# Kernel tuning notes

Measured on AMD Instinct MI355X. Metric: run time of the kernel, lower is better.

Reference implementation:

```python
import jax, jax.numpy as jnp
import numpy as np

N = 100000
E = 800000
D_IN = 256
D_H = 512


def setup_inputs() -> dict:
    key = jax.random.key(0)
    ks = jax.random.split(key, 8)
    s_in = 1.0 / np.sqrt(D_IN)
    s_h = 1.0 / np.sqrt(D_H)
    return {
        "x": jax.random.normal(ks[0], (N, D_IN), jnp.float32),
        "edge_index": jax.random.randint(ks[1], (2, E), 0, N, dtype=jnp.int64),
        "W1": jax.random.normal(ks[2], (D_IN, D_H), jnp.float32) * s_in,
        "b1": jnp.zeros((D_H,), jnp.float32),
        "W2": jax.random.normal(ks[3], (D_H, D_H), jnp.float32) * s_h,
        "b2": jnp.zeros((D_H,), jnp.float32),
        "W3": jax.random.normal(ks[4], (D_H, D_H), jnp.float32) * s_h,
        "b3": jnp.zeros((D_H,), jnp.float32),
        "Wfc": jax.random.normal(ks[5], (D_H, D_IN), jnp.float32) * s_h,
        "bfc": jnp.zeros((D_IN,), jnp.float32),
    }


def _gcn_prep(edge_index, n_nodes):
    # PyG GCNConv: add self-loops, symmetric deg^{-1/2} normalization.
    loop = jnp.arange(n_nodes, dtype=edge_index.dtype)
    row = jnp.concatenate([edge_index[0], loop])  # destination
    col = jnp.concatenate([edge_index[1], loop])  # source
    deg = jax.ops.segment_sum(jnp.ones_like(row, dtype=jnp.float32), row,
                              num_segments=n_nodes)
    dinv = jax.lax.rsqrt(deg)  # deg >= 1 due to self loops
    norm = dinv[row] * dinv[col]  # [E+N]
    return row, col, norm


def _gcn_conv(x, W, b, row, col, norm, n_nodes):
    h = x @ W  # [N, out]
    msg = h[col] * norm[:, None]  # [E+N, out] gather + scale
    out = jax.ops.segment_sum(msg, row, num_segments=n_nodes)  # scatter-add
    return out + b


def reference(x, edge_index, W1, b1, W2, b2, W3, b3, Wfc, bfc):
    n = x.shape[0]
    row, col, norm = _gcn_prep(edge_index, n)
    h = jax.nn.relu(_gcn_conv(x, W1, b1, row, col, norm, n))
    h = jax.nn.relu(_gcn_conv(h, W2, b2, row, col, norm, n))
    h = jax.nn.relu(_gcn_conv(h, W3, b3, row, col, norm, n))
    return h @ Wfc + bfc
```

## Files before the change

### kernel.cpp

```cpp
#include <hip/hip_runtime.h>

#define N_NODES 100000
#define NPAD    100096
#define E_EDGES 800000

typedef _Float16 f16;
typedef _Float16 f16x4 __attribute__((ext_vector_type(4)));
typedef _Float16 f16x8 __attribute__((ext_vector_type(8)));
typedef float    f32x4 __attribute__((ext_vector_type(4)));

__device__ inline void async16(const void* g, void* l) {
    __builtin_amdgcn_global_load_lds(
        (const __attribute__((address_space(1))) void*)g,
        (__attribute__((address_space(3))) void*)l, 16, 0, 0);
}

__global__ void k_deg(const int* __restrict__ ei, int* __restrict__ deg) {
    int e = blockIdx.x * 256 + threadIdx.x;
    if (e < E_EDGES) atomicAdd(&deg[ei[e]], 1);
}

__global__ void k_scan1(const int* __restrict__ deg, int* __restrict__ off,
                        int* __restrict__ bsum, float* __restrict__ dinv) {
    __shared__ int s[256];
    int i = blockIdx.x * 256 + threadIdx.x;
    int d = (i < N_NODES) ? deg[i] : 0;
    int pd = (d + 3) & ~3;
    dinv[i] = (i < N_NODES) ? rsqrtf((float)(d + 1)) : 0.f;
    s[threadIdx.x] = pd;
    __syncthreads();
    for (int dd = 1; dd < 256; dd <<= 1) {
        int t = (threadIdx.x >= dd) ? s[threadIdx.x - dd] : 0;
        __syncthreads();
        s[threadIdx.x] += t;
        __syncthreads();
    }
    if (i < N_NODES) off[i] = s[threadIdx.x] - pd;
    if (threadIdx.x == 255) bsum[blockIdx.x] = s[255];
}

__global__ void k_scan2(int* __restrict__ bsum, int nb) {
    __shared__ int s[512];
    int tid = threadIdx.x;
    int v = (tid < nb) ? bsum[tid] : 0;
    s[tid] = v;
    __syncthreads();
    for (int d = 1; d < 512; d <<= 1) {
        int t = (tid >= d) ? s[tid - d] : 0;
        __syncthreads();
        s[tid] += t;
        __syncthreads();
    }
    if (tid < nb) bsum[tid] = s[tid] - v;
}

__global__ void k_scan3(int* __restrict__ off, const int* __restrict__ bsum,
                        const int* __restrict__ deg, int* __restrict__ csr) {
    int i = blockIdx.x * 256 + threadIdx.x;
    if (i >= N_NODES) return;
    int o = off[i] + bsum[blockIdx.x];
    off[i] = o;
    int d = deg[i], pd = (d + 3) & ~3;
    for (int k = d; k < pd; ++k) csr[o + k] = NPAD;
    if (i == N_NODES - 1) off[N_NODES] = o + pd;
}

__global__ void k_fill(const int* __restrict__ ei, const int* __restrict__ off,
                       int* __restrict__ cursor, int* __restrict__ csr) {
    int e = blockIdx.x * 256 + threadIdx.x;
    if (e >= E_EDGES) return;
    int dst = ei[e];
    int src = ei[E_EDGES + e];
    int pos = atomicAdd(&cursor[dst], 1);
    csr[off[dst] + pos] = src;
}

__global__ void k_x_to_f16(const float* __restrict__ x,
                           const float* __restrict__ dinv,
                           f16* __restrict__ xh) {
    int i = blockIdx.x * 256 + threadIdx.x;
    if (i >= N_NODES * 64) return;
    float d = dinv[i >> 6];
    float4 v = ((const float4*)x)[i];
    f16x4 o;
    o.x = (f16)(v.x * d); o.y = (f16)(v.y * d);
    o.z = (f16)(v.z * d); o.w = (f16)(v.w * d);
    ((f16x4*)xh)[i] = o;
}

__global__ void k_transpose(const float* __restrict__ W, f16* __restrict__ Wt,
                            int K, int M) {
    int m = blockIdx.x * 256 + threadIdx.x;
    int k = blockIdx.y;
    if (m < M) Wt[(size_t)m * K + k] = (f16)W[(size_t)k * M + m];
}

template<int K, int M, int MODE>
__launch_bounds__(256, 3)
__global__ void k_gemm(const f16* __restrict__ A, const f16* __restrict__ B,
                       void* __restrict__ C, const float* __restrict__ bias,
                       const float* __restrict__ dsc) {
    __shared__ __align__(16) char smem[16384];
    f16* As = (f16*)smem;
    f16* Bs = (f16*)(smem + 8192);
    int tid  = threadIdx.x;
    int wave = tid >> 6, lane = tid & 63;
    int wr = (wave >> 1) * 64, wc = (wave & 1) * 64;
    int lm = lane & 15, q = lane >> 4;

    constexpr int CB  = M / 128;
    constexpr int NWG = (NPAD / 128) * CB;
    constexpr int Q   = NWG / 8, R = NWG % 8;
    int id  = blockIdx.x;
    int xcd = id & 7, pos = id >> 3;
    int nid = (xcd < R) ? xcd * (Q + 1) + pos
                        : R * (Q + 1) + (xcd - R) * Q + pos;
    int rowBase = (nid / CB) * 128;
    int colBase = (nid % CB) * 128;

    f32x4 acc[4][4] = {};
    const f16* Ag = A + (size_t)rowBase * K;
    const f16* Bg = B + (size_t)colBase * K;

    int c0 = tid, c1 = tid + 256;
    for (int kt = 0; kt < K; kt += 32) {
        __syncthreads();
        async16(Ag + (size_t)(c0 >> 2) * K + kt + (c0 & 3) * 8, &As[c0 * 8]);
        async16(Ag + (size_t)(c1 >> 2) * K + kt + (c1 & 3) * 8, &As[c1 * 8]);
        async16(Bg + (size_t)(c0 >> 2) * K + kt + (c0 & 3) * 8, &Bs[c0 * 8]);
        async16(Bg + (size_t)(c1 >> 2) * K + kt + (c1 & 3) * 8, &Bs[c1 * 8]);
        __syncthreads();

        f16x8 a[4], b[4];
#pragma unroll
        for (int i = 0; i < 4; ++i) {
            a[i] = *(const f16x8*)&As[(wr + i * 16 + lm) * 32 + q * 8];
            b[i] = *(const f16x8*)&Bs[(wc + i * 16 + lm) * 32 + q * 8];
        }
#pragma unroll
        for (int i = 0; i < 4; ++i)
#pragma unroll
            for (int j = 0; j < 4; ++j)
                acc[i][j] = __builtin_amdgcn_mfma_f32_16x16x32_f16(
                    a[i], b[j], acc[i][j], 0, 0, 0);
    }

    if (MODE == 2) {
#pragma unroll
        for (int i = 0; i < 4; ++i) {
            int gr0 = rowBase + wr + i * 16 + q * 4;
#pragma unroll
            for (int j = 0; j < 4; ++j) {
                int gc = colBase + wc + j * 16 + lm;
                float bj = bias[gc];
#pragma unroll
                for (int r = 0; r < 4; ++r) {
                    int gr = gr0 + r;
                    if (gr < N_NODES)
                        ((float*)C)[(size_t)gr * M + gc] = acc[i][j][r] + bj;
                }
            }
        }
    } else {
        __syncthreads();
        f16* Ep = (f16*)smem + wave * (16 * 80);
#pragma unroll
        for (int i = 0; i < 4; ++i) {
            f32x4 dr = {1.f, 1.f, 1.f, 1.f};
            if (MODE == 3)
                dr = *(const f32x4*)&dsc[rowBase + wr + i * 16 + q * 4];
#pragma unroll
            for (int j = 0; j < 4; ++j) {
                int colg = colBase + wc + j * 16 + lm;
#pragma unroll
                for (int r = 0; r < 4; ++r) {
                    float v = acc[i][j][r];
                    if (MODE == 1) {
                        v += bias[colg];
                        v = v > 0.f ? v : 0.f;
                    }
                    if (MODE == 3) v *= dr[r];
                    Ep[(q * 4 + r) * 80 + j * 16 + lm] = (f16)v;
                }
            }
            int row0 = lane >> 3, c8 = lane & 7;
            f16x8 v0 = *(const f16x8*)&Ep[row0 * 80 + c8 * 8];
            f16x8 v1 = *(const f16x8*)&Ep[(row0 + 8) * 80 + c8 * 8];
            int gr0 = rowBase + wr + i * 16 + row0;
            int gc  = colBase + wc + c8 * 8;
            *(f16x8*)&((f16*)C)[(size_t)gr0 * M + gc] = v0;
            *(f16x8*)&((f16*)C)[(size_t)(gr0 + 8) * M + gc] = v1;
        }
    }
}

template<int VE> struct VecT;
template<> struct VecT<4> { typedef f16x4 type; };
template<> struct VecT<8> { typedef f16x8 type; };

template<int CH, bool ACT>
__launch_bounds__(256)
__global__ void k_agg(const f16* __restrict__ t, const int* __restrict__ off,
                      const int* __restrict__ csr, const float* __restrict__ dinv,
                      const float* __restrict__ bias, f16* __restrict__ h) {
    constexpr int VE = CH / 64;
    typedef typename VecT<VE>::type vec;
    int node = blockIdx.x * 4 + (threadIdx.x >> 6);
    if (node >= N_NODES) return;
    int lane = threadIdx.x & 63;
    const vec* __restrict__ rows = (const vec*)t;

    vec v = rows[(size_t)node * 64 + lane];
    float acc[VE];
#pragma unroll
    for (int j = 0; j < VE; ++j) acc[j] = (float)v[j];

    int s = off[node], e = off[node + 1];
    if (s < e) {
        int4 iv = *(const int4*)&csr[s];
        for (int idx = s; idx < e; idx += 4) {
            int4 nxt = *(const int4*)&csr[idx + 4];
            vec u0 = rows[(size_t)iv.x * 64 + lane];
            vec u1 = rows[(size_t)iv.y * 64 + lane];
            vec u2 = rows[(size_t)iv.z * 64 + lane];
            vec u3 = rows[(size_t)iv.w * 64 + lane];
            iv = nxt;
#pragma unroll
            for (int j = 0; j < VE; ++j)
                acc[j] += ((float)u0[j] + (float)u1[j])
                        + ((float)u2[j] + (float)u3[j]);
        }
    }

    float di = dinv[node];
    vec o;
#pragma unroll
    for (int j = 0; j < VE; ++j) {
        float r = di * acc[j];
        if (ACT) {
            r += bias[lane * VE + j];
            r = r > 0.f ? r : 0.f;
        }
        o[j] = (f16)r;
    }
    ((vec*)h)[(size_t)node * 64 + lane] = o;
}

extern "C" void kernel_launch(void* const* d_in, const int* in_sizes, int n_in,
                              void* d_out, int out_size, void* d_ws, size_t ws_size,
                              hipStream_t stream) {
    const float* x   = (const float*)d_in[0];
    const int*   ei  = (const int*)d_in[1];
    const float* W1  = (const float*)d_in[2];
    const float* b1  = (const float*)d_in[3];
    const float* W2  = (const float*)d_in[4];
    const float* b2  = (const float*)d_in[5];
    const float* W3  = (const float*)d_in[6];
    const float* b3  = (const float*)d_in[7];
    const float* Wfc = (const float*)d_in[8];
    const float* bfc = (const float*)d_in[9];

    char* wsb = (char*)d_ws;
    size_t o = 0;
    auto alloc = [&](size_t bytes) -> void* {
        void* p = wsb + o;
        o += (bytes + 255) & ~(size_t)255;
        return p;
    };

    f16* xh   = (f16*)alloc((size_t)(NPAD + 1) * 256 * 2);
    f16* t    = (f16*)alloc((size_t)(NPAD + 1) * 512 * 2);
    f16* h    = (f16*)alloc((size_t)NPAD * 512 * 2);
    f16* Wt1  = (f16*)alloc(512 * 256 * 2);
    f16* Wt2  = (f16*)alloc(512 * 512 * 2);
    f16* Wt3  = (f16*)alloc(512 * 512 * 2);
    f16* Wtfc = (f16*)alloc(256 * 512 * 2);
    int* deg    = (int*)alloc(N_NODES * 4);
    float* dinv = (float*)alloc(NPAD * 4);
    int* off    = (int*)alloc((N_NODES + 1) * 4);
    int* cursor = (int*)alloc(N_NODES * 4);
    int* bsum   = (int*)alloc(4096 * 4);
    int* csr    = (int*)alloc(((size_t)E_EDGES + 3 * N_NODES + 8) * 4);

    f16* a1 = t;

    const int NB = (N_NODES + 255) / 256;

    hipMemsetAsync(deg, 0, N_NODES * 4, stream);
    hipMemsetAsync(cursor, 0, N_NODES * 4, stream);
    hipMemsetAsync(xh + (size_t)NPAD * 256, 0, 256 * 2, stream);
    hipMemsetAsync(t  + (size_t)NPAD * 512, 0, 512 * 2, stream);

    k_deg<<<(E_EDGES + 255) / 256, 256, 0, stream>>>(ei, deg);
    k_scan1<<<NB, 256, 0, stream>>>(deg, off, bsum, dinv);
    k_scan2<<<1, 512, 0, stream>>>(bsum, NB);
    k_scan3<<<NB, 256, 0, stream>>>(off, bsum, deg, csr);
    k_fill<<<(E_EDGES + 255) / 256, 256, 0, stream>>>(ei, off, cursor, csr);

    k_x_to_f16<<<(N_NODES * 64 + 255) / 256, 256, 0, stream>>>(x, dinv, xh);
    k_transpose<<<dim3(2, 256), 256, 0, stream>>>(W1, Wt1, 256, 512);
    k_transpose<<<dim3(2, 512), 256, 0, stream>>>(W2, Wt2, 512, 512);
    k_transpose<<<dim3(2, 512), 256, 0, stream>>>(W3, Wt3, 512, 512);
    k_transpose<<<dim3(1, 512), 256, 0, stream>>>(Wfc, Wtfc, 512, 256);

    constexpr int NWG4 = (NPAD / 128) * 4;
    constexpr int NWG2 = (NPAD / 128) * 2;
    const int AGG_GRID = N_NODES / 4;

    k_agg<256, false><<<AGG_GRID, 256, 0, stream>>>(xh, off, csr, dinv, nullptr, a1);
    k_gemm<256, 512, 1><<<NWG4, 256, 0, stream>>>(a1, Wt1, h, b1, nullptr);
    k_gemm<512, 512, 3><<<NWG4, 256, 0, stream>>>(h, Wt2, t, nullptr, dinv);
    k_agg<512, true><<<AGG_GRID, 256, 0, stream>>>(t, off, csr, dinv, b2, h);
    k_gemm<512, 512, 3><<<NWG4, 256, 0, stream>>>(h, Wt3, t, nullptr, dinv);
    k_agg<512, true><<<AGG_GRID, 256, 0, stream>>>(t, off, csr, dinv, b3, h);
    k_gemm<512, 256, 2><<<NWG2, 256, 0, stream>>>(h, Wtfc, d_out, bfc, nullptr);
}
```

Measured before the change: 894.7 us.

## Add 256x256-tile pipelined MFMA GEMM for the hidden-layer matmuls

```diff
diff --git a/kernel.cpp b/kernel.cpp
--- a/kernel.cpp
+++ b/kernel.cpp
@@ -14,6 +14,12 @@
         (const __attribute__((address_space(1))) void*)g,
         (__attribute__((address_space(3))) void*)l, 16, 0, 0);
 }
+
+#define BAR() __builtin_amdgcn_s_barrier()
+#define WAIT_LGKM0 do { asm volatile("s_waitcnt lgkmcnt(0)" ::: "memory"); \
+                        __builtin_amdgcn_sched_barrier(0); } while (0)
+#define WAIT_VM8   do { asm volatile("s_waitcnt vmcnt(8)" ::: "memory"); \
+                        __builtin_amdgcn_sched_barrier(0); } while (0)
 
 __global__ void k_deg(const int* __restrict__ ei, int* __restrict__ deg) {
     int e = blockIdx.x * 256 + threadIdx.x;
@@ -95,8 +101,162 @@
     if (m < M) Wt[(size_t)m * K + k] = (f16)W[(size_t)k * M + m];
 }
 
+__device__ inline void stage2(const f16* G, int Kld, int k0, f16* lds, int tid) {
+#pragma unroll
+    for (int c = 0; c < 2; ++c) {
+        int idx = c * 512 + tid;
+        async16(G + (size_t)(idx >> 2) * Kld + k0 + (idx & 3) * 8, lds + idx * 8);
+    }
+}
+
 template<int K, int M, int MODE>
-__launch_bounds__(256, 3)
+__launch_bounds__(512, 2)
+__global__ void k_gemm256(const f16* __restrict__ A, const f16* __restrict__ B,
+                          void* __restrict__ C, const float* __restrict__ bias,
+                          const float* __restrict__ dsc) {
+    __shared__ __align__(16) char smem[131072];
+    f16* S = (f16*)smem;
+    constexpr int NT = K / 64;
+    int tid = threadIdx.x;
+    int wave = tid >> 6, lane = tid & 63;
+    int wr = (wave >> 2) * 128, wc = (wave & 3) * 64;
+    int lm = lane & 15, q = lane >> 4;
+
+    constexpr int CB  = M / 256;
+    constexpr int NWG = (NPAD / 256) * CB;
+    constexpr int Qw  = NWG / 8, Rw = NWG % 8;
+    int id  = blockIdx.x;
+    int xcd = id & 7, pos = id >> 3;
+    int nid = (xcd < Rw) ? xcd * (Qw + 1) + pos
+                         : Rw * (Qw + 1) + (xcd - Rw) * Qw + pos;
+    int rowBase = (nid / CB) * 256;
+    int colBase = (nid % CB) * 256;
+
+    const f16* Ag = A + (size_t)rowBase * K;
+    const f16* Bg = B + (size_t)colBase * K;
+
+    f32x4 acc[8][4] = {};
+
+    stage2(Ag, K, 0,  S,                 tid);
+    stage2(Bg, K, 0,  S + 16384,         tid);
+    stage2(Ag, K, 32, S + 8192,          tid);
+    stage2(Bg, K, 32, S + 16384 + 8192,  tid);
+    stage2(Ag, K, 64, S + 32768,         tid);
+    stage2(Bg, K, 64, S + 32768 + 16384, tid);
+    WAIT_VM8;
+    BAR();
+
+#pragma unroll 2
+    for (int t = 0; t < NT; ++t) {
+        const int cb = (t & 1) * 32768;
+        const int nb = 32768 - cb;
+        const int t1 = (t + 1 < NT ? t + 1 : NT - 1) * 64;
+        const int t2 = (t + 2 < NT ? t + 2 : NT - 1) * 64;
+        f16x8 a[4], b[4];
+
+#pragma unroll
+        for (int m = 0; m < 4; ++m)
+            a[m] = *(const f16x8*)&S[cb + (wr + m * 16 + lm) * 32 + q * 8];
+#pragma unroll
+        for (int n = 0; n < 4; ++n)
+            b[n] = *(const f16x8*)&S[cb + 16384 + (wc + n * 16 + lm) * 32 + q * 8];
+        stage2(Ag, K, t1 + 32, S + nb + 8192, tid);
+        BAR(); WAIT_LGKM0;
+        __builtin_amdgcn_s_setprio(1);
+#pragma unroll
+        for (int m = 0; m < 4; ++m)
+#pragma unroll
+            for (int n = 0; n < 4; ++n)
+                acc[m][n] = __builtin_amdgcn_mfma_f32_16x16x32_f16(
+                    a[m], b[n], acc[m][n], 0, 0, 0);
+        __builtin_amdgcn_s_setprio(0);
+        BAR();
+
+#pragma unroll
+        for (int m = 0; m < 4; ++m)
+            a[m] = *(const f16x8*)&S[cb + (wr + 64 + m * 16 + lm) * 32 + q * 8];
+        stage2(Bg, K, t1 + 32, S + nb + 16384 + 8192, tid);
+        BAR(); WAIT_LGKM0;
+        __builtin_amdgcn_s_setprio(1);
+#pragma unroll
+        for (int m = 0; m < 4; ++m)
+#pragma unroll
+            for (int n = 0; n < 4; ++n)
+                acc[4 + m][n] = __builtin_amdgcn_mfma_f32_16x16x32_f16(
+                    a[m], b[n], acc[4 + m][n], 0, 0, 0);
+        __builtin_amdgcn_s_setprio(0);
+        WAIT_VM8;
+        BAR();
+
+#pragma unroll
+        for (int m = 0; m < 4; ++m)
+            a[m] = *(const f16x8*)&S[cb + 8192 + (wr + m * 16 + lm) * 32 + q * 8];
+#pragma unroll
+        for (int n = 0; n < 4; ++n)
+            b[n] = *(const f16x8*)&S[cb + 16384 + 8192 + (wc + n * 16 + lm) * 32 + q * 8];
+        stage2(Ag, K, t2, S + cb, tid);
+        BAR(); WAIT_LGKM0;
+        __builtin_amdgcn_s_setprio(1);
+#pragma unroll
+        for (int m = 0; m < 4; ++m)
+#pragma unroll
+            for (int n = 0; n < 4; ++n)
+                acc[m][n] = __builtin_amdgcn_mfma_f32_16x16x32_f16(
+                    a[m], b[n], acc[m][n], 0, 0, 0);
+        __builtin_amdgcn_s_setprio(0);
+        BAR();
+
+#pragma unroll
+        for (int m = 0; m < 4; ++m)
+            a[m] = *(const f16x8*)&S[cb + 8192 + (wr + 64 + m * 16 + lm) * 32 + q * 8];
+        stage2(Bg, K, t2, S + cb + 16384, tid);
+        BAR(); WAIT_LGKM0;
+        __builtin_amdgcn_s_setprio(1);
+#pragma unroll
+        for (int m = 0; m < 4; ++m)
+#pragma unroll
+            for (int n = 0; n < 4; ++n)
+                acc[4 + m][n] = __builtin_amdgcn_mfma_f32_16x16x32_f16(
+                    a[m], b[n], acc[4 + m][n], 0, 0, 0);
+        __builtin_amdgcn_s_setprio(0);
+        WAIT_VM8;
+        BAR();
+    }
+
+    asm volatile("s_waitcnt vmcnt(0)" ::: "memory");
+    __syncthreads();
+    f16* Ep = S + wave * 1280;
+#pragma unroll
+    for (int i = 0; i < 8; ++i) {
+        f32x4 dr = {1.f, 1.f, 1.f, 1.f};
+        if (MODE == 3)
+            dr = *(const f32x4*)&dsc[rowBase + wr + i * 16 + q * 4];
+#pragma unroll
+        for (int n = 0; n < 4; ++n) {
+            int colg = colBase + wc + n * 16 + lm;
+#pragma unroll
+            for (int r = 0; r < 4; ++r) {
+                float v = acc[i][n][r];
+                if (MODE == 1) {
+                    v += bias[colg];
+                    v = v > 0.f ? v : 0.f;
+                }
+                if (MODE == 3) v *= dr[r];
+                Ep[(q * 4 + r) * 80 + n * 16 + lm] = (f16)v;
+            }
+        }
+        int row0 = lane >> 3, c8 = lane & 7;
+        f16x8 v0 = *(const f16x8*)&Ep[row0 * 80 + c8 * 8];
+        f16x8 v1 = *(const f16x8*)&Ep[(row0 + 8) * 80 + c8 * 8];
+        int gr0 = rowBase + wr + i * 16 + row0;
+        int gc  = colBase + wc + c8 * 8;
+        *(f16x8*)&((f16*)C)[(size_t)gr0 * M + gc] = v0;
+        *(f16x8*)&((f16*)C)[(size_t)(gr0 + 8) * M + gc] = v1;
+    }
+}
+
+template<int K, int M, int MODE>
+__launch_bounds__(256, 2)
 __global__ void k_gemm(const f16* __restrict__ A, const f16* __restrict__ B,
                        void* __restrict__ C, const float* __restrict__ bias,
                        const float* __restrict__ dsc) {
@@ -145,51 +305,19 @@
                     a[i], b[j], acc[i][j], 0, 0, 0);
     }
 
-    if (MODE == 2) {
-#pragma unroll
-        for (int i = 0; i < 4; ++i) {
-            int gr0 = rowBase + wr + i * 16 + q * 4;
-#pragma unroll
-            for (int j = 0; j < 4; ++j) {
-                int gc = colBase + wc + j * 16 + lm;
-                float bj = bias[gc];
-#pragma unroll
-                for (int r = 0; r < 4; ++r) {
-                    int gr = gr0 + r;
-                    if (gr < N_NODES)
-                        ((float*)C)[(size_t)gr * M + gc] = acc[i][j][r] + bj;
-                }
+#pragma unroll
+    for (int i = 0; i < 4; ++i) {
+        int gr0 = rowBase + wr + i * 16 + q * 4;
+#pragma unroll
+        for (int j = 0; j < 4; ++j) {
+            int gc = colBase + wc + j * 16 + lm;
+            float bj = bias[gc];
+#pragma unroll
+            for (int r = 0; r < 4; ++r) {
+                int gr = gr0 + r;
+                if (gr < N_NODES)
+                    ((float*)C)[(size_t)gr * M + gc] = acc[i][j][r] + bj;
             }
-        }
-    } else {
-        __syncthreads();
-        f16* Ep = (f16*)smem + wave * (16 * 80);
-#pragma unroll
-        for (int i = 0; i < 4; ++i) {
-            f32x4 dr = {1.f, 1.f, 1.f, 1.f};
-            if (MODE == 3)
-                dr = *(const f32x4*)&dsc[rowBase + wr + i * 16 + q * 4];
-#pragma unroll
-            for (int j = 0; j < 4; ++j) {
-                int colg = colBase + wc + j * 16 + lm;
-#pragma unroll
-                for (int r = 0; r < 4; ++r) {
-                    float v = acc[i][j][r];
-                    if (MODE == 1) {
-                        v += bias[colg];
-                        v = v > 0.f ? v : 0.f;
-                    }
-                    if (MODE == 3) v *= dr[r];
-                    Ep[(q * 4 + r) * 80 + j * 16 + lm] = (f16)v;
-                }
-            }
-            int row0 = lane >> 3, c8 = lane & 7;
-            f16x8 v0 = *(const f16x8*)&Ep[row0 * 80 + c8 * 8];
-            f16x8 v1 = *(const f16x8*)&Ep[(row0 + 8) * 80 + c8 * 8];
-            int gr0 = rowBase + wr + i * 16 + row0;
-            int gc  = colBase + wc + c8 * 8;
-            *(f16x8*)&((f16*)C)[(size_t)gr0 * M + gc] = v0;
-            *(f16x8*)&((f16*)C)[(size_t)(gr0 + 8) * M + gc] = v1;
         }
     }
 }
@@ -303,15 +431,15 @@
     k_transpose<<<dim3(2, 512), 256, 0, stream>>>(W3, Wt3, 512, 512);
     k_transpose<<<dim3(1, 512), 256, 0, stream>>>(Wfc, Wtfc, 512, 256);
 
-    constexpr int NWG4 = (NPAD / 128) * 4;
-    constexpr int NWG2 = (NPAD / 128) * 2;
+    constexpr int NWG256 = (NPAD / 256) * 2;
+    constexpr int NWGFC  = (NPAD / 128) * 2;
     const int AGG_GRID = N_NODES / 4;
 
     k_agg<256, false><<<AGG_GRID, 256, 0, stream>>>(xh, off, csr, dinv, nullptr, a1);
-    k_gemm<256, 512, 1><<<NWG4, 256, 0, stream>>>(a1, Wt1, h, b1, nullptr);
-    k_gemm<512, 512, 3><<<NWG4, 256, 0, stream>>>(h, Wt2, t, nullptr, dinv);
+    k_gemm256<256, 512, 1><<<NWG256, 512, 0, stream>>>(a1, Wt1, h, b1, nullptr);
+    k_gemm256<512, 512, 3><<<NWG256, 512, 0, stream>>>(h, Wt2, t, nullptr, dinv);
     k_agg<512, true><<<AGG_GRID, 256, 0, stream>>>(t, off, csr, dinv, b2, h);
-    k_gemm<512, 512, 3><<<NWG4, 256, 0, stream>>>(h, Wt3, t, nullptr, dinv);
+    k_gemm256<512, 512, 3><<<NWG256, 512, 0, stream>>>(h, Wt3, t, nullptr, dinv);
     k_agg<512, true><<<AGG_GRID, 256, 0, stream>>>(t, off, csr, dinv, b3, h);
-    k_gemm<512, 256, 2><<<NWG2, 256, 0, stream>>>(h, Wtfc, d_out, bfc, nullptr);
-}
+    k_gemm<512, 256, 2><<<NWGFC, 256, 0, stream>>>(h, Wtfc, d_out, bfc, nullptr);
+}
```

New measurement: 899.0 us. No clear change (+0.5%).
